# Kernel tuning notes

Hardware: AMD Instinct MI355X
Metric: run time of the kernel (lower is better)

The kernel has to match this reference:

```python
import jax, jax.numpy as jnp
import numpy as np

EMBED = 1024
B, T = 4, 2048

def setup_inputs() -> dict:
    key = jax.random.key(0)
    k1, k2, k3, k4, k5 = jax.random.split(key, 5)
    s_in = 1.0 / np.sqrt(EMBED)
    return {
        "x": jax.random.normal(k1, (B, T, EMBED), dtype=jnp.float32),
        "w_qkv": jax.random.normal(k2, (3 * EMBED, EMBED), dtype=jnp.float32) * s_in,  # torch Linear layout [out,in]
        "b_qkv": jax.random.normal(k3, (3 * EMBED,), dtype=jnp.float32) * 0.01,
        "w_proj": jax.random.normal(k4, (EMBED, EMBED), dtype=jnp.float32) * s_in,
        "b_proj": jax.random.normal(k5, (EMBED,), dtype=jnp.float32) * 0.01,
    }

def reference(x, w_qkv, b_qkv, w_proj, b_proj):
    Bq, Tq, C = x.shape
    qkv = jnp.einsum('btc,oc->bto', x, w_qkv) + b_qkv        # [B,T,3C]
    q, k, v = jnp.split(qkv, 3, axis=-1)                      # each [B,T,C]
    att = jnp.einsum('btc,bsc->bts', q, k) / jnp.sqrt(jnp.float32(C))  # [B,T,T]
    causal = jnp.tril(jnp.ones((Tq, Tq), dtype=bool))
    att = jnp.where(causal[None, :, :], att, -jnp.inf)
    att = jax.nn.softmax(att, axis=-1)
    out = jnp.einsum('bts,bsc->btc', att, v)                   # [B,T,C]
    return jnp.einsum('btc,oc->bto', out, w_proj) + b_proj
```

## Files before the change

kernel.cpp:

```cpp
#include <hip/hip_runtime.h>
#include <hip/hip_bf16.h>

typedef __hip_bfloat16 bf16;
typedef __attribute__((ext_vector_type(8))) short bf16x8;
typedef __attribute__((ext_vector_type(4))) float f32x4;

#define GLD16(gp, lp) __builtin_amdgcn_global_load_lds( \
    (const __attribute__((address_space(1))) void*)(gp), \
    (__attribute__((address_space(3))) void*)(lp), 16, 0, 0)

__global__ __launch_bounds__(256) void cvt_bf16(const float* __restrict__ in,
                                                bf16* __restrict__ out) {
    int i = (blockIdx.x * 256 + threadIdx.x) * 4;
    float4 f = *(const float4*)&in[i];
    __hip_bfloat162 p0, p1;
    p0.x = __float2bfloat16(f.x); p0.y = __float2bfloat16(f.y);
    p1.x = __float2bfloat16(f.z); p1.y = __float2bfloat16(f.w);
    *(__hip_bfloat162*)&out[i]     = p0;
    *(__hip_bfloat162*)&out[i + 2] = p1;
}

__global__ void transpose_v(const bf16* __restrict__ V, bf16* __restrict__ Vt) {
    __shared__ bf16 tile[32][33];
    const int b = blockIdx.z;
    const int c0 = blockIdx.x * 32, t0 = blockIdx.y * 32;
    const int tx = threadIdx.x, ty = threadIdx.y;
    #pragma unroll
    for (int i = 0; i < 32; i += 8)
        tile[ty + i][tx] = V[((size_t)(b * 2048 + t0 + ty + i)) * 1024 + c0 + tx];
    __syncthreads();
    #pragma unroll
    for (int i = 0; i < 32; i += 8)
        Vt[((size_t)b * 1024 + c0 + ty + i) * 2048 + t0 + tx] = tile[tx][ty + i];
}

__global__ __launch_bounds__(256) void softmax_causal(float* __restrict__ S) {
    const int row = blockIdx.x;
    const int t = row & 2047;
    float* srow = S + (size_t)row * 2048;
    bf16* prow = (bf16*)srow;
    const int tid = threadIdx.x;
    const int base = tid * 8;
    float4 f0 = *(const float4*)&srow[base];
    float4 f1 = *(const float4*)&srow[base + 4];
    float v[8] = {f0.x, f0.y, f0.z, f0.w, f1.x, f1.y, f1.z, f1.w};
    float lmax = -INFINITY;
    #pragma unroll
    for (int i = 0; i < 8; ++i) {
        v[i] = (base + i <= t) ? v[i] : -INFINITY;
        lmax = fmaxf(lmax, v[i]);
    }
    #pragma unroll
    for (int off = 32; off; off >>= 1) lmax = fmaxf(lmax, __shfl_xor(lmax, off));
    __shared__ float red[4];
    const int wave = tid >> 6, lane = tid & 63;
    if (lane == 0) red[wave] = lmax;
    __syncthreads();
    lmax = fmaxf(fmaxf(red[0], red[1]), fmaxf(red[2], red[3]));
    float lsum = 0.f;
    #pragma unroll
    for (int i = 0; i < 8; ++i) { v[i] = __expf(v[i] - lmax); lsum += v[i]; }
    #pragma unroll
    for (int off = 32; off; off >>= 1) lsum += __shfl_xor(lsum, off);
    __syncthreads();
    if (lane == 0) red[wave] = lsum;
    __syncthreads();
    lsum = red[0] + red[1] + red[2] + red[3];
    const float inv = 1.f / lsum;
    #pragma unroll
    for (int i = 0; i < 8; ++i) prow[base + i] = __float2bfloat16(v[i] * inv);
}

__global__ __launch_bounds__(256) void gemm_bt(
    int mode,
    const bf16* __restrict__ A, int lda, size_t batchA,
    const bf16* __restrict__ B, int ldb, size_t batchB,
    int K,
    const float* __restrict__ bias,
    void* __restrict__ out0, void* __restrict__ out1, void* __restrict__ out2)
{
    constexpr int BK = 32;
    __shared__ bf16 As[128][BK];
    __shared__ bf16 Bs[128][BK];

    const int bx = blockIdx.x, by = blockIdx.y, bz = blockIdx.z;
    if (mode == 1 && bx > by) return;
    const int m0 = by * 128, n0 = bx * 128;
    const int keff = (mode == 2) ? (by + 1) * 128 : K;

    const bf16* Ab = A + (size_t)bz * batchA;
    const bf16* Bb = B + (size_t)bz * batchB;

    const int tid = threadIdx.x;
    const int lane = tid & 63;
    const int wave = tid >> 6;
    const int wm = (wave >> 1) * 64;
    const int wn = (wave & 1) * 64;

    f32x4 acc[4][4] = {};

    for (int k0 = 0; k0 < keff; k0 += BK) {
        #pragma unroll
        for (int p = 0; p < 2; ++p) {
            int idx = p * 256 + tid;
            int r = idx >> 2;
            int kc = (idx & 3) * 8;
            GLD16(Ab + (size_t)(m0 + r) * lda + (k0 + kc), &As[r][kc]);
            GLD16(Bb + (size_t)(n0 + r) * ldb + (k0 + kc), &Bs[r][kc]);
        }
        __syncthreads();

        bf16x8 af[4], bfr[4];
        #pragma unroll
        for (int m = 0; m < 4; ++m)
            af[m] = *(const bf16x8*)&As[wm + m * 16 + (lane & 15)][(lane >> 4) * 8];
        #pragma unroll
        for (int n = 0; n < 4; ++n)
            bfr[n] = *(const bf16x8*)&Bs[wn + n * 16 + (lane & 15)][(lane >> 4) * 8];
        #pragma unroll
        for (int m = 0; m < 4; ++m)
            #pragma unroll
            for (int n = 0; n < 4; ++n)
                acc[m][n] = __builtin_amdgcn_mfma_f32_16x16x32_bf16(
                    af[m], bfr[n], acc[m][n], 0, 0, 0);
        __syncthreads();
    }

    #pragma unroll
    for (int m = 0; m < 4; ++m) {
        #pragma unroll
        for (int n = 0; n < 4; ++n) {
            #pragma unroll
            for (int j = 0; j < 4; ++j) {
                const int gr = m0 + wm + m * 16 + ((lane >> 4) << 2) + j;
                const int gc = n0 + wn + n * 16 + (lane & 15);
                float v = acc[m][n][j];
                if (mode == 0) {
                    v += bias[gc];
                    const int which = gc >> 10;
                    const int col = gc & 1023;
                    bf16* dst = which == 0 ? (bf16*)out0
                              : which == 1 ? (bf16*)out1 : (bf16*)out2;
                    dst[(size_t)gr * 1024 + col] = __float2bfloat16(v);
                } else if (mode == 1) {
                    ((float*)out0)[(size_t)bz * (2048ull * 2048) +
                                   (size_t)gr * 2048 + gc] = v * 0.03125f;
                } else if (mode == 2) {
                    ((bf16*)out0)[((size_t)bz * 2048 + gr) * 1024 + gc] =
                        __float2bfloat16(v);
                } else {
                    ((float*)out0)[(size_t)gr * 1024 + gc] = v + bias[gc];
                }
            }
        }
    }
}

template<int MODE>
__global__ __launch_bounds__(512, 2) void gemm256(
    const bf16* __restrict__ A, const bf16* __restrict__ B,
    const float* __restrict__ bias,
    void* __restrict__ out0, void* __restrict__ out1, void* __restrict__ out2)
{
    __shared__ bf16 As[2][256][64];
    __shared__ bf16 Bs[2][256][64];
    constexpr int NT = 16;

    const int bx = blockIdx.x, by = blockIdx.y, bz = blockIdx.z;
    if (MODE == 1 && bx > by) return;
    const int m0 = by * 256, n0 = bx * 256;

    const bf16* Ab = A + (MODE == 1 ? (size_t)bz * (2048ull * 1024) : 0);
    const bf16* Bb = B + (MODE == 1 ? (size_t)bz * (2048ull * 1024) : 0);

    const int tid = threadIdx.x;
    const int lane = tid & 63, wave = tid >> 6;
    const int wr = wave >> 2, wc = wave & 3;
    const int frow = lane & 15, fk = lane >> 4, fx = lane & 7;

    const int rl = tid >> 3;
    const int scol = ((tid & 7) ^ (rl & 7)) * 8;
    const bf16* pAsrc = Ab + (size_t)(m0 + rl) * 1024 + scol;
    const bf16* pBsrc = Bb + (size_t)(n0 + rl) * 1024 + scol;
    const int dchunk = tid * 8;

    f32x4 acc[4][4][2] = {};

    #define STG(P, LDSBASE, H, K0) do { \
        GLD16((P) + (size_t)(H) * 128 * 1024 + (K0), (LDSBASE) + (H) * 8192 + dchunk); \
        GLD16((P) + (size_t)((H) * 128 + 64) * 1024 + (K0), (LDSBASE) + (H) * 8192 + 4096 + dchunk); \
    } while (0)

    {
        bf16* la = &As[0][0][0]; bf16* lb = &Bs[0][0][0];
        STG(pAsrc, la, 0, 0);
        STG(pBsrc, lb, 0, 0);
        STG(pBsrc, lb, 1, 0);
        STG(pAsrc, la, 1, 0);
    }

    for (int t = 0; t < NT; ++t) {
        const int buf = t & 1, nbuf = buf ^ 1;
        const int kn = (t + 1) * 64;
        bf16* lan = &As[nbuf][0][0]; bf16* lbn = &Bs[nbuf][0][0];
        const bool more = (t + 1 < NT);

        #pragma unroll
        for (int q = 0; q < 4; ++q) {
            if (more) {
                if (q == 0)      STG(pAsrc, lan, 0, kn);
                else if (q == 1) STG(pBsrc, lbn, 0, kn);
                else if (q == 2) STG(pBsrc, lbn, 1, kn);
                else             STG(pAsrc, lan, 1, kn);
                if (q < 3) asm volatile("s_waitcnt vmcnt(6)" ::: "memory");
            } else {
                if (q == 0)      asm volatile("s_waitcnt vmcnt(4)" ::: "memory");
                else if (q == 1) asm volatile("s_waitcnt vmcnt(2)" ::: "memory");
                else if (q == 2) asm volatile("s_waitcnt vmcnt(0)" ::: "memory");
            }
            __builtin_amdgcn_s_barrier();

            const int aR = ((q >> 1) << 7) + wr * 64 + frow;
            const int bR = ((q & 1) << 7) + wc * 32 + frow;
            bf16x8 av[4][2], bv[2][2];
            #pragma unroll
            for (int m = 0; m < 4; ++m)
                #pragma unroll
                for (int ks = 0; ks < 2; ++ks)
                    av[m][ks] = *(const bf16x8*)
                        &As[buf][aR + m * 16][((((ks << 2) | fk) ^ fx) << 3)];
            #pragma unroll
            for (int n = 0; n < 2; ++n)
                #pragma unroll
                for (int ks = 0; ks < 2; ++ks)
                    bv[n][ks] = *(const bf16x8*)
                        &Bs[buf][bR + n * 16][((((ks << 2) | fk) ^ fx) << 3)];

            __builtin_amdgcn_s_setprio(1);
            #pragma unroll
            for (int m = 0; m < 4; ++m)
                #pragma unroll
                for (int n = 0; n < 2; ++n)
                    #pragma unroll
                    for (int ks = 0; ks < 2; ++ks)
                        acc[q][m][n] = __builtin_amdgcn_mfma_f32_16x16x32_bf16(
                            av[m][ks], bv[n][ks], acc[q][m][n], 0, 0, 0);
            __builtin_amdgcn_s_setprio(0);
        }
    }
    #undef STG

    #pragma unroll
    for (int q = 0; q < 4; ++q) {
        #pragma unroll
        for (int m = 0; m < 4; ++m) {
            #pragma unroll
            for (int n = 0; n < 2; ++n) {
                #pragma unroll
                for (int j = 0; j < 4; ++j) {
                    const int gr = m0 + ((q >> 1) << 7) + wr * 64 + m * 16 + (fk << 2) + j;
                    const int gc = n0 + ((q & 1) << 7) + wc * 32 + n * 16 + frow;
                    float v = acc[q][m][n][j];
                    if (MODE == 0) {
                        v += bias[gc];
                        const int which = gc >> 10;
                        const int col = gc & 1023;
                        bf16* dst = which == 0 ? (bf16*)out0
                                  : which == 1 ? (bf16*)out1 : (bf16*)out2;
                        dst[(size_t)gr * 1024 + col] = __float2bfloat16(v);
                    } else if (MODE == 1) {
                        ((float*)out0)[(size_t)bz * (2048ull * 2048) +
                                       (size_t)gr * 2048 + gc] = v * 0.03125f;
                    } else {
                        ((float*)out0)[(size_t)gr * 1024 + gc] = v + bias[gc];
                    }
                }
            }
        }
    }
}

extern "C" void kernel_launch(void* const* d_in, const int* in_sizes, int n_in,
                              void* d_out, int out_size, void* d_ws, size_t ws_size,
                              hipStream_t stream) {
    const float* x      = (const float*)d_in[0];
    const float* w_qkv  = (const float*)d_in[1];
    const float* b_qkv  = (const float*)d_in[2];
    const float* w_proj = (const float*)d_in[3];
    const float* b_proj = (const float*)d_in[4];
    float* out = (float*)d_out;
    char* ws = (char*)d_ws;

    bf16* Xb = (bf16*)(ws);
    bf16* Wq = (bf16*)(ws + 16777216);
    bf16* Wp = (bf16*)(ws + 23068672);
    bf16* Qb = (bf16*)(ws + 25165824);
    bf16* Kb = (bf16*)(ws + 41943040);
    bf16* Vb = (bf16*)(ws + 58720256);
    float* S = (float*)(ws + 75497472);
    bf16* Vt = Xb;
    bf16* O  = Qb;

    hipLaunchKernelGGL(cvt_bf16, dim3(8192), dim3(256), 0, stream, x, Xb);
    hipLaunchKernelGGL(cvt_bf16, dim3(3072), dim3(256), 0, stream, w_qkv, Wq);
    hipLaunchKernelGGL(cvt_bf16, dim3(1024), dim3(256), 0, stream, w_proj, Wp);

    gemm256<0><<<dim3(12, 32, 1), 512, 0, stream>>>(
        Xb, Wq, b_qkv, (void*)Qb, (void*)Kb, (void*)Vb);

    hipLaunchKernelGGL(transpose_v, dim3(32, 64, 4), dim3(32, 8), 0, stream, Vb, Vt);

    gemm256<1><<<dim3(8, 8, 4), 512, 0, stream>>>(
        Qb, Kb, (const float*)nullptr, (void*)S, nullptr, nullptr);

    hipLaunchKernelGGL(softmax_causal, dim3(8192), dim3(256), 0, stream, S);

    hipLaunchKernelGGL(gemm_bt, dim3(8, 16, 4), dim3(256), 0, stream,
        2, (const bf16*)S, 4096, (size_t)(2048ull * 4096), Vt, 2048,
        (size_t)(1024ull * 2048), 2048, (const float*)nullptr,
        (void*)O, (void*)nullptr, (void*)nullptr);

    gemm256<3><<<dim3(4, 32, 1), 512, 0, stream>>>(
        O, Wp, b_proj, (void*)out, nullptr, nullptr);
}
```

Baseline: 339.1 us.

## Route PV GEMM through gemm256, restructure pipeline barriers, merge weight conversion

Replaces the simple 128x128 gemm_bt used for the attention-times-V product with a MODE 2 instance of the 256x256 double-buffered gemm256, using causal K truncation and the stride differences of S and Vt. The gemm256 main loop is reordered so LDS fragment reads come before the next-stage global loads, with barriers and waitcnts placed after the MFMA block to overlap loads with compute. The two weight conversion launches are merged into one kernel. The aim is higher MFMA efficiency on the PV GEMM and less launch overhead. The risks are load imbalance from the causal tile sizes and hazards from the new synchronization order.

```diff
diff --git a/kernel.cpp b/kernel.cpp
--- a/kernel.cpp
+++ b/kernel.cpp
@@ -12,6 +12,22 @@
 __global__ __launch_bounds__(256) void cvt_bf16(const float* __restrict__ in,
                                                 bf16* __restrict__ out) {
     int i = (blockIdx.x * 256 + threadIdx.x) * 4;
+    float4 f = *(const float4*)&in[i];
+    __hip_bfloat162 p0, p1;
+    p0.x = __float2bfloat16(f.x); p0.y = __float2bfloat16(f.y);
+    p1.x = __float2bfloat16(f.z); p1.y = __float2bfloat16(f.w);
+    *(__hip_bfloat162*)&out[i]     = p0;
+    *(__hip_bfloat162*)&out[i + 2] = p1;
+}
+
+__global__ __launch_bounds__(256) void cvt_weights(
+    const float* __restrict__ wq, bf16* __restrict__ wqo,
+    const float* __restrict__ wp, bf16* __restrict__ wpo) {
+    int blk = blockIdx.x;
+    const float* in; bf16* out; int base;
+    if (blk < 3072) { in = wq; out = wqo; base = blk; }
+    else            { in = wp; out = wpo; base = blk - 3072; }
+    int i = (base * 256 + threadIdx.x) * 4;
     float4 f = *(const float4*)&in[i];
     __hip_bfloat162 p0, p1;
     p0.x = __float2bfloat16(f.x); p0.y = __float2bfloat16(f.y);
@@ -71,91 +87,6 @@
     for (int i = 0; i < 8; ++i) prow[base + i] = __float2bfloat16(v[i] * inv);
 }
 
-__global__ __launch_bounds__(256) void gemm_bt(
-    int mode,
-    const bf16* __restrict__ A, int lda, size_t batchA,
-    const bf16* __restrict__ B, int ldb, size_t batchB,
-    int K,
-    const float* __restrict__ bias,
-    void* __restrict__ out0, void* __restrict__ out1, void* __restrict__ out2)
-{
-    constexpr int BK = 32;
-    __shared__ bf16 As[128][BK];
-    __shared__ bf16 Bs[128][BK];
-
-    const int bx = blockIdx.x, by = blockIdx.y, bz = blockIdx.z;
-    if (mode == 1 && bx > by) return;
-    const int m0 = by * 128, n0 = bx * 128;
-    const int keff = (mode == 2) ? (by + 1) * 128 : K;
-
-    const bf16* Ab = A + (size_t)bz * batchA;
-    const bf16* Bb = B + (size_t)bz * batchB;
-
-    const int tid = threadIdx.x;
-    const int lane = tid & 63;
-    const int wave = tid >> 6;
-    const int wm = (wave >> 1) * 64;
-    const int wn = (wave & 1) * 64;
-
-    f32x4 acc[4][4] = {};
-
-    for (int k0 = 0; k0 < keff; k0 += BK) {
-        #pragma unroll
-        for (int p = 0; p < 2; ++p) {
-            int idx = p * 256 + tid;
-            int r = idx >> 2;
-            int kc = (idx & 3) * 8;
-            GLD16(Ab + (size_t)(m0 + r) * lda + (k0 + kc), &As[r][kc]);
-            GLD16(Bb + (size_t)(n0 + r) * ldb + (k0 + kc), &Bs[r][kc]);
-        }
-        __syncthreads();
-
-        bf16x8 af[4], bfr[4];
-        #pragma unroll
-        for (int m = 0; m < 4; ++m)
-            af[m] = *(const bf16x8*)&As[wm + m * 16 + (lane & 15)][(lane >> 4) * 8];
-        #pragma unroll
-        for (int n = 0; n < 4; ++n)
-            bfr[n] = *(const bf16x8*)&Bs[wn + n * 16 + (lane & 15)][(lane >> 4) * 8];
-        #pragma unroll
-        for (int m = 0; m < 4; ++m)
-            #pragma unroll
-            for (int n = 0; n < 4; ++n)
-                acc[m][n] = __builtin_amdgcn_mfma_f32_16x16x32_bf16(
-                    af[m], bfr[n], acc[m][n], 0, 0, 0);
-        __syncthreads();
-    }
-
-    #pragma unroll
-    for (int m = 0; m < 4; ++m) {
-        #pragma unroll
-        for (int n = 0; n < 4; ++n) {
-            #pragma unroll
-            for (int j = 0; j < 4; ++j) {
-                const int gr = m0 + wm + m * 16 + ((lane >> 4) << 2) + j;
-                const int gc = n0 + wn + n * 16 + (lane & 15);
-                float v = acc[m][n][j];
-                if (mode == 0) {
-                    v += bias[gc];
-                    const int which = gc >> 10;
-                    const int col = gc & 1023;
-                    bf16* dst = which == 0 ? (bf16*)out0
-                              : which == 1 ? (bf16*)out1 : (bf16*)out2;
-                    dst[(size_t)gr * 1024 + col] = __float2bfloat16(v);
-                } else if (mode == 1) {
-                    ((float*)out0)[(size_t)bz * (2048ull * 2048) +
-                                   (size_t)gr * 2048 + gc] = v * 0.03125f;
-                } else if (mode == 2) {
-                    ((bf16*)out0)[((size_t)bz * 2048 + gr) * 1024 + gc] =
-                        __float2bfloat16(v);
-                } else {
-                    ((float*)out0)[(size_t)gr * 1024 + gc] = v + bias[gc];
-                }
-            }
-        }
-    }
-}
-
 template<int MODE>
 __global__ __launch_bounds__(512, 2) void gemm256(
     const bf16* __restrict__ A, const bf16* __restrict__ B,
@@ -164,14 +95,18 @@
 {
     __shared__ bf16 As[2][256][64];
     __shared__ bf16 Bs[2][256][64];
-    constexpr int NT = 16;
+    constexpr int LDA = (MODE == 2) ? 4096 : 1024;
+    constexpr int LDB = (MODE == 2) ? 2048 : 1024;
 
     const int bx = blockIdx.x, by = blockIdx.y, bz = blockIdx.z;
     if (MODE == 1 && bx > by) return;
+    const int NT = (MODE == 2) ? 4 * (by + 1) : 16;
     const int m0 = by * 256, n0 = bx * 256;
 
-    const bf16* Ab = A + (MODE == 1 ? (size_t)bz * (2048ull * 1024) : 0);
-    const bf16* Bb = B + (MODE == 1 ? (size_t)bz * (2048ull * 1024) : 0);
+    const bf16* Ab = A;
+    const bf16* Bb = B;
+    if (MODE == 1) { Ab += (size_t)bz * (2048ull * 1024); Bb += (size_t)bz * (2048ull * 1024); }
+    if (MODE == 2) { Ab += (size_t)bz * (2048ull * 4096); Bb += (size_t)bz * (1024ull * 2048); }
 
     const int tid = threadIdx.x;
     const int lane = tid & 63, wave = tid >> 6;
@@ -180,23 +115,25 @@
 
     const int rl = tid >> 3;
     const int scol = ((tid & 7) ^ (rl & 7)) * 8;
-    const bf16* pAsrc = Ab + (size_t)(m0 + rl) * 1024 + scol;
-    const bf16* pBsrc = Bb + (size_t)(n0 + rl) * 1024 + scol;
+    const bf16* pAsrc = Ab + (size_t)(m0 + rl) * LDA + scol;
+    const bf16* pBsrc = Bb + (size_t)(n0 + rl) * LDB + scol;
     const int dchunk = tid * 8;
 
     f32x4 acc[4][4][2] = {};
 
-    #define STG(P, LDSBASE, H, K0) do { \
-        GLD16((P) + (size_t)(H) * 128 * 1024 + (K0), (LDSBASE) + (H) * 8192 + dchunk); \
-        GLD16((P) + (size_t)((H) * 128 + 64) * 1024 + (K0), (LDSBASE) + (H) * 8192 + 4096 + dchunk); \
+    #define STG(P, LD, LDSBASE, H, K0) do { \
+        GLD16((P) + (size_t)(H) * 128 * (LD) + (K0), (LDSBASE) + (H) * 8192 + dchunk); \
+        GLD16((P) + (size_t)((H) * 128 + 64) * (LD) + (K0), (LDSBASE) + (H) * 8192 + 4096 + dchunk); \
     } while (0)
 
     {
         bf16* la = &As[0][0][0]; bf16* lb = &Bs[0][0][0];
-        STG(pAsrc, la, 0, 0);
-        STG(pBsrc, lb, 0, 0);
-        STG(pBsrc, lb, 1, 0);
-        STG(pAsrc, la, 1, 0);
+        STG(pAsrc, LDA, la, 0, 0);
+        STG(pBsrc, LDB, lb, 0, 0);
+        STG(pBsrc, LDB, lb, 1, 0);
+        STG(pAsrc, LDA, la, 1, 0);
+        asm volatile("s_waitcnt vmcnt(4)" ::: "memory");
+        __builtin_amdgcn_s_barrier();
     }
 
     for (int t = 0; t < NT; ++t) {
@@ -207,19 +144,6 @@
 
         #pragma unroll
         for (int q = 0; q < 4; ++q) {
-            if (more) {
-                if (q == 0)      STG(pAsrc, lan, 0, kn);
-                else if (q == 1) STG(pBsrc, lbn, 0, kn);
-                else if (q == 2) STG(pBsrc, lbn, 1, kn);
-                else             STG(pAsrc, lan, 1, kn);
-                if (q < 3) asm volatile("s_waitcnt vmcnt(6)" ::: "memory");
-            } else {
-                if (q == 0)      asm volatile("s_waitcnt vmcnt(4)" ::: "memory");
-                else if (q == 1) asm volatile("s_waitcnt vmcnt(2)" ::: "memory");
-                else if (q == 2) asm volatile("s_waitcnt vmcnt(0)" ::: "memory");
-            }
-            __builtin_amdgcn_s_barrier();
-
             const int aR = ((q >> 1) << 7) + wr * 64 + frow;
             const int bR = ((q & 1) << 7) + wc * 32 + frow;
             bf16x8 av[4][2], bv[2][2];
@@ -235,6 +159,18 @@
                 for (int ks = 0; ks < 2; ++ks)
                     bv[n][ks] = *(const bf16x8*)
                         &Bs[buf][bR + n * 16][((((ks << 2) | fk) ^ fx) << 3)];
+
+            if (more) {
+                if (q == 0)      STG(pAsrc, LDA, lan, 0, kn);
+                else if (q == 1) STG(pBsrc, LDB, lbn, 0, kn);
+                else if (q == 2) STG(pBsrc, LDB, lbn, 1, kn);
+                else             STG(pAsrc, LDA, lan, 1, kn);
+            }
+
+            __builtin_amdgcn_sched_barrier(0);
+            __builtin_amdgcn_s_barrier();
+            asm volatile("s_waitcnt lgkmcnt(0)" ::: "memory");
+            __builtin_amdgcn_sched_barrier(0);
 
             __builtin_amdgcn_s_setprio(1);
             #pragma unroll
@@ -246,6 +182,15 @@
                         acc[q][m][n] = __builtin_amdgcn_mfma_f32_16x16x32_bf16(
                             av[m][ks], bv[n][ks], acc[q][m][n], 0, 0, 0);
             __builtin_amdgcn_s_setprio(0);
+            __builtin_amdgcn_sched_barrier(0);
+
+            if (more) {
+                if (q != 2) asm volatile("s_waitcnt vmcnt(4)" ::: "memory");
+            } else {
+                if (q == 0)      asm volatile("s_waitcnt vmcnt(2)" ::: "memory");
+                else if (q == 1) asm volatile("s_waitcnt vmcnt(0)" ::: "memory");
+            }
+            __builtin_amdgcn_s_barrier();
         }
     }
     #undef STG
@@ -271,6 +216,9 @@
                     } else if (MODE == 1) {
                         ((float*)out0)[(size_t)bz * (2048ull * 2048) +
                                        (size_t)gr * 2048 + gc] = v * 0.03125f;
+                    } else if (MODE == 2) {
+                        ((bf16*)out0)[((size_t)bz * 2048 + gr) * 1024 + gc] =
+                            __float2bfloat16(v);
                     } else {
                         ((float*)out0)[(size_t)gr * 1024 + gc] = v + bias[gc];
                     }
@@ -302,8 +250,8 @@
     bf16* O  = Qb;
 
     hipLaunchKernelGGL(cvt_bf16, dim3(8192), dim3(256), 0, stream, x, Xb);
-    hipLaunchKernelGGL(cvt_bf16, dim3(3072), dim3(256), 0, stream, w_qkv, Wq);
-    hipLaunchKernelGGL(cvt_bf16, dim3(1024), dim3(256), 0, stream, w_proj, Wp);
+    hipLaunchKernelGGL(cvt_weights, dim3(4096), dim3(256), 0, stream,
+                       w_qkv, Wq, w_proj, Wp);
 
     gemm256<0><<<dim3(12, 32, 1), 512, 0, stream>>>(
         Xb, Wq, b_qkv, (void*)Qb, (void*)Kb, (void*)Vb);
@@ -315,10 +263,8 @@
 
     hipLaunchKernelGGL(softmax_causal, dim3(8192), dim3(256), 0, stream, S);
 
-    hipLaunchKernelGGL(gemm_bt, dim3(8, 16, 4), dim3(256), 0, stream,
-        2, (const bf16*)S, 4096, (size_t)(2048ull * 4096), Vt, 2048,
-        (size_t)(1024ull * 2048), 2048, (const float*)nullptr,
-        (void*)O, (void*)nullptr, (void*)nullptr);
+    gemm256<2><<<dim3(4, 8, 4), 512, 0, stream>>>(
+        (const bf16*)S, Vt, (const float*)nullptr, (void*)O, nullptr, nullptr);
 
     gemm256<3><<<dim3(4, 32, 1), 512, 0, stream>>>(
         O, Wp, b_proj, (void*)out, nullptr, nullptr);
```

After: 364.9 us. +7.6%, slower.
